# Kernel optimization log

Measured on AMD Instinct MI355X. Metric: run time of the kernel, lower is better.

Reference implementation:

```python
import jax, jax.numpy as jnp
import numpy as np

B, S, E = 2, 2048, 1024
HID = 1024
HEADS = 16
EPS = 1e-5
SCALE = (E * 2) ** (-0.5)  # source uses input_data_dim*2


def setup_inputs() -> dict:
    key = jax.random.key(0)
    k1, k2, k3 = jax.random.split(key, 3)
    return {
        "x": jax.random.normal(k1, (B, S, E), dtype=jnp.float32),
        "ln_g": jnp.ones((E,), jnp.float32),
        "ln_b": jnp.zeros((E,), jnp.float32),
        "W1": jax.random.normal(k2, (E, 3 * HID), jnp.float32) * 0.02,
        "b1": jnp.zeros((3 * HID,), jnp.float32),
        "W2": jax.random.normal(k3, (HID, HID), jnp.float32) * 0.02,
        "b2": jnp.zeros((HID,), jnp.float32),
    }


def reference(x, ln_g, ln_b, W1, b1, W2, b2):
    # LayerNorm over last dim
    mu = jnp.mean(x, axis=-1, keepdims=True)
    var = jnp.mean(jnp.square(x - mu), axis=-1, keepdims=True)
    xn = (x - mu) * jax.lax.rsqrt(var + EPS) * ln_g + ln_b
    # QKV projection: [B,S,3*HID]
    qkv = jnp.einsum('bse,ef->bsf', xn, W1) + b1
    # Faithful to source: flat reshape to (heads, B, S, 3*HID/heads)
    qkv_heads = qkv.reshape(HEADS, B, S, -1)
    q, k, v = jnp.split(qkv_heads, 3, axis=-1)  # each [H,B,S,d]
    scores = jnp.einsum('hbse,hbSe->hbsS', q, k) * SCALE  # [H,B,S,S]
    att = jax.nn.softmax(scores, axis=-1)
    full_att = jnp.einsum('hbsS,hbSe->hbse', att, v)  # [H,B,S,d]
    full_att = full_att.reshape(B, S, -1)  # faithful flat reshape -> [B,S,HID]
    out = jnp.einsum('bsh,hk->bsk', full_att, W2) + b2
    return out
```

## Files before the change

kernel.cpp:

```cpp
#include <hip/hip_runtime.h>

typedef unsigned short u16;
typedef __bf16 bf16x8 __attribute__((ext_vector_type(8)));
typedef float f32x4 __attribute__((ext_vector_type(4)));

static constexpr float SCALE2 = 0.022097086912079608f * 1.4426950408889634f;

__device__ __forceinline__ u16 f2b(float f) {
  union { float f; unsigned int i; } v; v.f = f;
  unsigned int r = v.i + 0x7fffu + ((v.i >> 16) & 1u);
  return (u16)(r >> 16);
}
__device__ __forceinline__ void async16(const u16* g, u16* l) {
  __builtin_amdgcn_global_load_lds((const __attribute__((address_space(1))) void*)g,
                                   (__attribute__((address_space(3))) void*)l,
                                   16, 0, 0);
}

__global__ __launch_bounds__(256) void ln_kernel(const float* __restrict__ x,
                                                 const float* __restrict__ g,
                                                 const float* __restrict__ b,
                                                 u16* __restrict__ xn) {
  const int row = blockIdx.x;
  const int t = threadIdx.x;
  float4 v = *(const float4*)(x + (size_t)row * 1024 + t * 4);
  float s = v.x + v.y + v.z + v.w;
  float ss = v.x * v.x + v.y * v.y + v.z * v.z + v.w * v.w;
  for (int off = 32; off >= 1; off >>= 1) {
    s += __shfl_xor(s, off, 64);
    ss += __shfl_xor(ss, off, 64);
  }
  __shared__ float red[8];
  const int w = t >> 6;
  if ((t & 63) == 0) { red[w] = s; red[4 + w] = ss; }
  __syncthreads();
  s = red[0] + red[1] + red[2] + red[3];
  ss = red[4] + red[5] + red[6] + red[7];
  const float mu = s * (1.0f / 1024.0f);
  const float var = ss * (1.0f / 1024.0f) - mu * mu;
  const float inv = rsqrtf(var + 1e-5f);
  float4 gg = *(const float4*)(g + t * 4);
  float4 bb = *(const float4*)(b + t * 4);
  ushort4 o;
  o.x = f2b((v.x - mu) * inv * gg.x + bb.x);
  o.y = f2b((v.y - mu) * inv * gg.y + bb.y);
  o.z = f2b((v.z - mu) * inv * gg.z + bb.z);
  o.w = f2b((v.w - mu) * inv * gg.w + bb.w);
  *(ushort4*)(xn + (size_t)row * 1024 + t * 4) = o;
}

__global__ void transpose_k(const float* __restrict__ in, u16* __restrict__ out,
                            int R, int C) {
  __shared__ float tile[32][33];
  const int c0 = blockIdx.x * 32, r0 = blockIdx.y * 32;
  const int tx = threadIdx.x, ty = threadIdx.y;
  for (int i = 0; i < 32; i += 8)
    tile[ty + i][tx] = in[(size_t)(r0 + ty + i) * C + c0 + tx];
  __syncthreads();
  for (int i = 0; i < 32; i += 8)
    out[(size_t)(c0 + ty + i) * R + r0 + tx] = f2b(tile[tx][ty + i]);
}

template <int MODE, int MT>
__global__ __launch_bounds__(256) void gemm_bt(const u16* __restrict__ A,
                                               const u16* __restrict__ Bt,
                                               const float* __restrict__ bias,
                                               float* __restrict__ C,
                                               int M, int N, int K,
                                               u16* __restrict__ Qc,
                                               u16* __restrict__ Kc,
                                               u16* __restrict__ Vtmp) {
  __shared__ __align__(16) u16 SMEM[8192];
  u16* As = SMEM;
  u16* Bs = SMEM + MT * 32;
  const int m0 = blockIdx.y * MT, n0 = blockIdx.x * 128;
  const int t = threadIdx.x, w = t >> 6, lane = t & 63;
  const int q = lane >> 4, l16 = lane & 15;
  const int wm = (w >> 1) * (MT / 2), wn = (w & 1) * 64;
  constexpr int NI = MT / 32;

  const int sc = (lane & 3) ^ ((lane >> 3) & 3);
  const u16* ap = A + (size_t)(m0 + w * 16 + (lane >> 2)) * K + sc * 8;
  const u16* bp = Bt + (size_t)(n0 + w * 16 + (lane >> 2)) * K + sc * 8;
  u16* lA = &As[w * 512];
  u16* lB = &Bs[w * 512];
  const int ac = q ^ ((l16 >> 1) & 3);

  f32x4 acc[NI][4];
  const f32x4 zero = {0.f, 0.f, 0.f, 0.f};
  for (int i = 0; i < NI; i++)
    for (int j = 0; j < 4; j++) acc[i][j] = zero;

  for (int k0 = 0; k0 < K; k0 += 32) {
    for (int i = 0; i < MT / 64; i++)
      async16(ap + (size_t)(i * 64) * K, lA + i * 2048);
    for (int i = 0; i < 2; i++)
      async16(bp + (size_t)(i * 64) * K, lB + i * 2048);
    ap += 32; bp += 32;
    __syncthreads();
    bf16x8 af[NI], bfr[4];
    for (int i = 0; i < NI; i++)
      af[i] = *(const bf16x8*)&As[(wm + i * 16 + l16) * 32 + ac * 8];
    for (int j = 0; j < 4; j++)
      bfr[j] = *(const bf16x8*)&Bs[(wn + j * 16 + l16) * 32 + ac * 8];
    for (int i = 0; i < NI; i++)
      for (int j = 0; j < 4; j++)
        acc[i][j] = __builtin_amdgcn_mfma_f32_16x16x32_bf16(af[i], bfr[j], acc[i][j], 0, 0, 0);
    __syncthreads();
  }

  if constexpr (MODE == 0) {
    for (int j = 0; j < 4; j++) {
      const int col = n0 + wn + j * 16 + l16;
      const float bv = bias[col];
      for (int i = 0; i < NI; i++) {
        const int rbase = m0 + wm + i * 16 + q * 4;
        for (int r = 0; r < 4; r++)
          C[(size_t)(rbase + r) * N + col] = acc[i][j][r] + bv;
      }
    }
  } else {
    const int seg = n0 + wn;
    const int k64 = seg >> 6;
    const int tcol = k64 / 3;
    const int typ = k64 - tcol * 3;
    u16* dst = (typ == 0) ? Qc : (typ == 1) ? Kc : Vtmp;
    const int gidx = m0 >> 7;
    u16* tw = &SMEM[w * 1280];
    float bv[4];
    for (int j = 0; j < 4; j++) bv[j] = bias[seg + j * 16 + l16];
    __syncthreads();
    for (int i = 0; i < 4; i++) {
      for (int j = 0; j < 4; j++) {
        ushort4 pk;
        pk.x = f2b(acc[i][j][0] + bv[j]);
        pk.y = f2b(acc[i][j][1] + bv[j]);
        pk.z = f2b(acc[i][j][2] + bv[j]);
        pk.w = f2b(acc[i][j][3] + bv[j]);
        *(ushort4*)&tw[(j * 16 + l16) * 20 + q * 4] = pk;
      }
      const int r2 = lane >> 2;
      const int quarter = lane & 3;
      u16 vals[16];
      for (int c = 0; c < 16; c++)
        vals[c] = tw[(quarter * 16 + c) * 20 + r2];
      const int lr = wm + i * 16 + r2;
      const int s = (lr << 4) + tcol;
      u16* dp = dst + ((size_t)gidx * 2048 + s) * 64 + quarter * 16;
      *(uint4*)&dp[0] = *(uint4*)&vals[0];
      *(uint4*)&dp[8] = *(uint4*)&vals[8];
    }
  }
}

__global__ __launch_bounds__(256) void vtrans(const u16* __restrict__ Vtmp,
                                              u16* __restrict__ Vt) {
  __shared__ __align__(16) u16 tile[64 * 64];
  const int g = blockIdx.y, s0 = blockIdx.x * 64;
  const int t = threadIdx.x;
  const int row = t >> 3, ch = t & 7;
  for (int p = 0; p < 2; p++) {
    const int r = p * 32 + row;
    uint4 v = *(const uint4*)&Vtmp[((size_t)g * 2048 + s0 + r) * 64 + ch * 8];
    *(uint4*)&tile[r * 64 + ((ch ^ (r & 7)) * 8)] = v;
  }
  __syncthreads();
  const int d = t >> 2, scn = t & 3;
  u16 vals[16];
  for (int j2 = 0; j2 < 16; j2++) {
    const int s = scn * 16 + j2;
    vals[j2] = tile[s * 64 + (((d >> 3) ^ (s & 7)) * 8) + (d & 7)];
  }
  u16* dp = Vt + ((size_t)g * 64 + d) * 2048 + s0 + scn * 16;
  *(uint4*)&dp[0] = *(uint4*)&vals[0];
  *(uint4*)&dp[8] = *(uint4*)&vals[8];
}

__global__ __launch_bounds__(256) void attn_kernel(const u16* __restrict__ Qc,
                                                   const u16* __restrict__ Kc,
                                                   const u16* __restrict__ Vt,
                                                   u16* __restrict__ Oc) {
  __shared__ __align__(16) u16 Ks[128 * 64];
  __shared__ __align__(16) u16 Ps[4 * 2176];
  __shared__ __align__(16) u16 Vs[64 * 128];
  const int g = blockIdx.y;
  const int q0 = blockIdx.x * 64;
  const int t = threadIdx.x, w = t >> 6, lane = t & 63;
  const int q = lane >> 4, l16 = lane & 15;

  const u16* Qg = Qc + (size_t)g * 2048 * 64;
  const u16* Kg = Kc + (size_t)g * 2048 * 64;
  const u16* Vg = Vt + (size_t)g * 64 * 2048;

  bf16x8 aq[2];
  for (int ks = 0; ks < 2; ks++)
    aq[ks] = *(const bf16x8*)&Qg[(size_t)(q0 + w * 16 + l16) * 64 + ks * 32 + q * 8];

  f32x4 accO[4];
  const f32x4 zero = {0.f, 0.f, 0.f, 0.f};
  for (int c = 0; c < 4; c++) accO[c] = zero;
  float m2 = -1e30f, lsum = 0.f;

  const int kc = (lane & 7) ^ ((lane >> 3) & 7);
  const int vc = (lane & 15) ^ ((w * 4 + (lane >> 4)) & 7);
  const u16* kp = Kg + (size_t)(w * 8 + (lane >> 3)) * 64 + kc * 8;
  const u16* vp = Vg + (size_t)(w * 4 + (lane >> 4)) * 2048 + vc * 8;
  u16* lK = &Ks[w * 512];
  u16* lV = &Vs[w * 512];

  const int kch = q ^ (l16 & 7);

  for (int it = 0; it < 16; it++) {
    const int kt0 = it * 128;
    for (int i = 0; i < 4; i++) {
      async16(kp + (size_t)kt0 * 64 + i * 2048, lK + i * 2048);
      async16(vp + kt0 + (size_t)i * 32768, lV + i * 2048);
    }
    __syncthreads();

    f32x4 sa[8];
    for (int ct = 0; ct < 8; ct++) {
      bf16x8 bk0 = *(const bf16x8*)&Ks[(ct * 16 + l16) * 64 + kch * 8];
      bf16x8 bk1 = *(const bf16x8*)&Ks[(ct * 16 + l16) * 64 + (kch ^ 4) * 8];
      f32x4 a = zero;
      a = __builtin_amdgcn_mfma_f32_16x16x32_bf16(bk0, aq[0], a, 0, 0, 0);
      a = __builtin_amdgcn_mfma_f32_16x16x32_bf16(bk1, aq[1], a, 0, 0, 0);
      sa[ct] = a;
    }

    float mx = -1e30f;
    for (int ct = 0; ct < 8; ct++) {
      sa[ct] *= SCALE2;
      for (int r = 0; r < 4; r++) mx = fmaxf(mx, sa[ct][r]);
    }
    mx = fmaxf(mx, __shfl_xor(mx, 16, 64));
    mx = fmaxf(mx, __shfl_xor(mx, 32, 64));
    const float mnew = fmaxf(m2, mx);
    const float alpha = __builtin_amdgcn_exp2f(m2 - mnew);
    m2 = mnew;

    u16* Pr = &Ps[w * 2176 + l16 * 136];
    f32x4 psv = zero;
    for (int ct = 0; ct < 8; ct++) {
      f32x4 p;
      for (int r = 0; r < 4; r++) p[r] = __builtin_amdgcn_exp2f(sa[ct][r] - mnew);
      psv += p;
      ushort4 pk;
      pk.x = f2b(p[0]); pk.y = f2b(p[1]); pk.z = f2b(p[2]); pk.w = f2b(p[3]);
      *(ushort4*)&Pr[ct * 16 + q * 4] = pk;
    }
    float psum = psv[0] + psv[1] + psv[2] + psv[3];
    psum += __shfl_xor(psum, 16, 64);
    psum += __shfl_xor(psum, 32, 64);
    lsum = lsum * alpha + psum;
    for (int c = 0; c < 4; c++) accO[c] *= alpha;

    u16* Psw = &Ps[w * 2176];
    for (int ks2 = 0; ks2 < 4; ks2++) {
      bf16x8 apf = *(const bf16x8*)&Psw[l16 * 136 + ks2 * 32 + q * 8];
      for (int c = 0; c < 4; c++) {
        const int vch = (ks2 * 4 + q) ^ (l16 & 7);
        bf16x8 bv = *(const bf16x8*)&Vs[(c * 16 + l16) * 128 + vch * 8];
        accO[c] = __builtin_amdgcn_mfma_f32_16x16x32_bf16(bv, apf, accO[c], 0, 0, 0);
      }
    }
    __syncthreads();
  }

  const int srow = q0 + w * 16 + l16;
  const int orow = g * 128 + (srow >> 4);
  const int cbase = (srow & 15) * 64;
  const float linv = 1.0f / lsum;
  for (int c = 0; c < 4; c++) {
    ushort4 o;
    o.x = f2b(accO[c][0] * linv);
    o.y = f2b(accO[c][1] * linv);
    o.z = f2b(accO[c][2] * linv);
    o.w = f2b(accO[c][3] * linv);
    *(ushort4*)&Oc[(size_t)orow * 1024 + cbase + c * 16 + q * 4] = o;
  }
}

extern "C" void kernel_launch(void* const* d_in, const int* in_sizes, int n_in,
                              void* d_out, int out_size, void* d_ws, size_t ws_size,
                              hipStream_t stream) {
  (void)in_sizes; (void)n_in; (void)out_size; (void)ws_size;
  const float* x    = (const float*)d_in[0];
  const float* ln_g = (const float*)d_in[1];
  const float* ln_b = (const float*)d_in[2];
  const float* W1   = (const float*)d_in[3];
  const float* b1   = (const float*)d_in[4];
  const float* W2   = (const float*)d_in[5];
  const float* b2   = (const float*)d_in[6];

  char* ws = (char*)d_ws;
  u16* xn   = (u16*)(ws);
  u16* W1T  = (u16*)(ws + ((size_t)8 << 20));
  u16* W2T  = (u16*)(ws + ((size_t)14 << 20));
  u16* Qc   = (u16*)(ws + ((size_t)16 << 20));
  u16* Kc   = (u16*)(ws + ((size_t)24 << 20));
  u16* Vtmp = (u16*)(ws + ((size_t)32 << 20));
  u16* Vt   = (u16*)(ws + ((size_t)40 << 20));
  u16* Oc   = xn;

  ln_kernel<<<dim3(4096), dim3(256), 0, stream>>>(x, ln_g, ln_b, xn);
  transpose_k<<<dim3(96, 32), dim3(32, 8), 0, stream>>>(W1, W1T, 1024, 3072);
  transpose_k<<<dim3(32, 32), dim3(32, 8), 0, stream>>>(W2, W2T, 1024, 1024);
  gemm_bt<1, 128><<<dim3(24, 32), dim3(256), 0, stream>>>(xn, W1T, b1, nullptr,
                                                          4096, 3072, 1024, Qc, Kc, Vtmp);
  vtrans<<<dim3(32, 32), dim3(256), 0, stream>>>(Vtmp, Vt);
  attn_kernel<<<dim3(32, 32), dim3(256), 0, stream>>>(Qc, Kc, Vt, Oc);
  gemm_bt<0, 64><<<dim3(8, 64), dim3(256), 0, stream>>>(Oc, W2T, b2, (float*)d_out,
                                                        4096, 1024, 1024, nullptr, nullptr, nullptr);
}
```

Baseline: 230.8 us.

## Double query rows per attention block and merge weight transposes into one kernel

```diff
diff --git a/kernel.cpp b/kernel.cpp
--- a/kernel.cpp
+++ b/kernel.cpp
@@ -49,16 +49,32 @@
   *(ushort4*)(xn + (size_t)row * 1024 + t * 4) = o;
 }
 
-__global__ void transpose_k(const float* __restrict__ in, u16* __restrict__ out,
-                            int R, int C) {
-  __shared__ float tile[32][33];
-  const int c0 = blockIdx.x * 32, r0 = blockIdx.y * 32;
-  const int tx = threadIdx.x, ty = threadIdx.y;
-  for (int i = 0; i < 32; i += 8)
-    tile[ty + i][tx] = in[(size_t)(r0 + ty + i) * C + c0 + tx];
+__global__ __launch_bounds__(256) void transpose2_k(const float* __restrict__ W1,
+                                                    u16* __restrict__ W1T,
+                                                    const float* __restrict__ W2,
+                                                    u16* __restrict__ W2T) {
+  const int z = blockIdx.z;
+  if (z == 1 && blockIdx.x >= 16) return;
+  const int C = z ? 1024 : 3072;
+  const float* in = z ? W2 : W1;
+  u16* out = z ? W2T : W1T;
+  __shared__ u16 tile[64 * 72];
+  const int c0 = blockIdx.x * 64, r0 = blockIdx.y * 64;
+  const int t = threadIdx.x;
+  const int row = t >> 2, cseg = t & 3;
+  for (int it = 0; it < 4; it++) {
+    float4 v = *(const float4*)&in[(size_t)(r0 + row) * C + c0 + it * 16 + cseg * 4];
+    ushort4 o;
+    o.x = f2b(v.x); o.y = f2b(v.y); o.z = f2b(v.z); o.w = f2b(v.w);
+    *(ushort4*)&tile[row * 72 + it * 16 + cseg * 4] = o;
+  }
   __syncthreads();
-  for (int i = 0; i < 32; i += 8)
-    out[(size_t)(c0 + ty + i) * R + r0 + tx] = f2b(tile[tx][ty + i]);
+  const int orow = t >> 2, ch = t & 3;
+  u16 vals[16];
+  for (int j = 0; j < 16; j++) vals[j] = tile[(ch * 16 + j) * 72 + orow];
+  u16* dp = out + (size_t)(c0 + orow) * 1024 + r0 + ch * 16;
+  *(uint4*)&dp[0] = *(uint4*)&vals[0];
+  *(uint4*)&dp[8] = *(uint4*)&vals[8];
 }
 
 template <int MODE, int MT>
@@ -180,11 +196,12 @@
                                                    const u16* __restrict__ Kc,
                                                    const u16* __restrict__ Vt,
                                                    u16* __restrict__ Oc) {
-  __shared__ __align__(16) u16 Ks[128 * 64];
-  __shared__ __align__(16) u16 Ps[4 * 2176];
-  __shared__ __align__(16) u16 Vs[64 * 128];
+  __shared__ __align__(16) u16 LDS[32768];
+  u16* Ks = LDS;
+  u16* Vs = LDS + 8192;
+  u16* Ps = LDS + 16384;
   const int g = blockIdx.y;
-  const int q0 = blockIdx.x * 64;
+  const int q0 = blockIdx.x * 128;
   const int t = threadIdx.x, w = t >> 6, lane = t & 63;
   const int q = lane >> 4, l16 = lane & 15;
 
@@ -192,14 +209,16 @@
   const u16* Kg = Kc + (size_t)g * 2048 * 64;
   const u16* Vg = Vt + (size_t)g * 64 * 2048;
 
-  bf16x8 aq[2];
-  for (int ks = 0; ks < 2; ks++)
-    aq[ks] = *(const bf16x8*)&Qg[(size_t)(q0 + w * 16 + l16) * 64 + ks * 32 + q * 8];
-
-  f32x4 accO[4];
+  bf16x8 aq[2][2];
+  for (int rt = 0; rt < 2; rt++)
+    for (int ks = 0; ks < 2; ks++)
+      aq[rt][ks] = *(const bf16x8*)&Qg[(size_t)(q0 + w * 32 + rt * 16 + l16) * 64 + ks * 32 + q * 8];
+
+  f32x4 accO[2][4];
   const f32x4 zero = {0.f, 0.f, 0.f, 0.f};
-  for (int c = 0; c < 4; c++) accO[c] = zero;
-  float m2 = -1e30f, lsum = 0.f;
+  for (int rt = 0; rt < 2; rt++)
+    for (int c = 0; c < 4; c++) accO[rt][c] = zero;
+  float m2[2] = {-1e30f, -1e30f}, lsum[2] = {0.f, 0.f};
 
   const int kc = (lane & 7) ^ ((lane >> 3) & 7);
   const int vc = (lane & 15) ^ ((w * 4 + (lane >> 4)) & 7);
@@ -209,6 +228,8 @@
   u16* lV = &Vs[w * 512];
 
   const int kch = q ^ (l16 & 7);
+  const int pbase = w * 4096;
+  const int pxor = l16 & 3;
 
   for (int it = 0; it < 16; it++) {
     const int kt0 = it * 128;
@@ -218,66 +239,74 @@
     }
     __syncthreads();
 
-    f32x4 sa[8];
+    f32x4 sa[2][8];
     for (int ct = 0; ct < 8; ct++) {
       bf16x8 bk0 = *(const bf16x8*)&Ks[(ct * 16 + l16) * 64 + kch * 8];
       bf16x8 bk1 = *(const bf16x8*)&Ks[(ct * 16 + l16) * 64 + (kch ^ 4) * 8];
-      f32x4 a = zero;
-      a = __builtin_amdgcn_mfma_f32_16x16x32_bf16(bk0, aq[0], a, 0, 0, 0);
-      a = __builtin_amdgcn_mfma_f32_16x16x32_bf16(bk1, aq[1], a, 0, 0, 0);
-      sa[ct] = a;
-    }
-
-    float mx = -1e30f;
-    for (int ct = 0; ct < 8; ct++) {
-      sa[ct] *= SCALE2;
-      for (int r = 0; r < 4; r++) mx = fmaxf(mx, sa[ct][r]);
-    }
-    mx = fmaxf(mx, __shfl_xor(mx, 16, 64));
-    mx = fmaxf(mx, __shfl_xor(mx, 32, 64));
-    const float mnew = fmaxf(m2, mx);
-    const float alpha = __builtin_amdgcn_exp2f(m2 - mnew);
-    m2 = mnew;
-
-    u16* Pr = &Ps[w * 2176 + l16 * 136];
-    f32x4 psv = zero;
-    for (int ct = 0; ct < 8; ct++) {
-      f32x4 p;
-      for (int r = 0; r < 4; r++) p[r] = __builtin_amdgcn_exp2f(sa[ct][r] - mnew);
-      psv += p;
-      ushort4 pk;
-      pk.x = f2b(p[0]); pk.y = f2b(p[1]); pk.z = f2b(p[2]); pk.w = f2b(p[3]);
-      *(ushort4*)&Pr[ct * 16 + q * 4] = pk;
-    }
-    float psum = psv[0] + psv[1] + psv[2] + psv[3];
-    psum += __shfl_xor(psum, 16, 64);
-    psum += __shfl_xor(psum, 32, 64);
-    lsum = lsum * alpha + psum;
-    for (int c = 0; c < 4; c++) accO[c] *= alpha;
-
-    u16* Psw = &Ps[w * 2176];
+      for (int rt = 0; rt < 2; rt++) {
+        f32x4 a = zero;
+        a = __builtin_amdgcn_mfma_f32_16x16x32_bf16(bk0, aq[rt][0], a, 0, 0, 0);
+        a = __builtin_amdgcn_mfma_f32_16x16x32_bf16(bk1, aq[rt][1], a, 0, 0, 0);
+        sa[rt][ct] = a;
+      }
+    }
+
+    for (int rt = 0; rt < 2; rt++) {
+      float mx = -1e30f;
+      for (int ct = 0; ct < 8; ct++) {
+        sa[rt][ct] *= SCALE2;
+        for (int r = 0; r < 4; r++) mx = fmaxf(mx, sa[rt][ct][r]);
+      }
+      mx = fmaxf(mx, __shfl_xor(mx, 16, 64));
+      mx = fmaxf(mx, __shfl_xor(mx, 32, 64));
+      const float mnew = fmaxf(m2[rt], mx);
+      const float alpha = __builtin_amdgcn_exp2f(m2[rt] - mnew);
+      m2[rt] = mnew;
+      const int sbase = pbase + rt * 2048 + l16 * 32;
+      f32x4 psv = zero;
+      for (int ct = 0; ct < 8; ct++) {
+        f32x4 p;
+        for (int r = 0; r < 4; r++) p[r] = __builtin_amdgcn_exp2f(sa[rt][ct][r] - mnew);
+        psv += p;
+        ushort4 pk;
+        pk.x = f2b(p[0]); pk.y = f2b(p[1]); pk.z = f2b(p[2]); pk.w = f2b(p[3]);
+        const int c2 = ((ct & 1) * 2 + (q >> 1)) ^ pxor;
+        *(ushort4*)&Ps[sbase + (ct >> 1) * 512 + c2 * 8 + (q & 1) * 4] = pk;
+      }
+      float psum = psv[0] + psv[1] + psv[2] + psv[3];
+      psum += __shfl_xor(psum, 16, 64);
+      psum += __shfl_xor(psum, 32, 64);
+      lsum[rt] = lsum[rt] * alpha + psum;
+      for (int c = 0; c < 4; c++) accO[rt][c] *= alpha;
+    }
+
     for (int ks2 = 0; ks2 < 4; ks2++) {
-      bf16x8 apf = *(const bf16x8*)&Psw[l16 * 136 + ks2 * 32 + q * 8];
+      bf16x8 apf[2];
+      for (int rt = 0; rt < 2; rt++)
+        apf[rt] = *(const bf16x8*)&Ps[pbase + rt * 2048 + ks2 * 512 + l16 * 32 + (ks2 * 0 + (q ^ pxor)) * 8];
       for (int c = 0; c < 4; c++) {
         const int vch = (ks2 * 4 + q) ^ (l16 & 7);
         bf16x8 bv = *(const bf16x8*)&Vs[(c * 16 + l16) * 128 + vch * 8];
-        accO[c] = __builtin_amdgcn_mfma_f32_16x16x32_bf16(bv, apf, accO[c], 0, 0, 0);
-      }
-    }
-    __syncthreads();
-  }
-
-  const int srow = q0 + w * 16 + l16;
-  const int orow = g * 128 + (srow >> 4);
-  const int cbase = (srow & 15) * 64;
-  const float linv = 1.0f / lsum;
-  for (int c = 0; c < 4; c++) {
-    ushort4 o;
-    o.x = f2b(accO[c][0] * linv);
-    o.y = f2b(accO[c][1] * linv);
-    o.z = f2b(accO[c][2] * linv);
-    o.w = f2b(accO[c][3] * linv);
-    *(ushort4*)&Oc[(size_t)orow * 1024 + cbase + c * 16 + q * 4] = o;
+        for (int rt = 0; rt < 2; rt++)
+          accO[rt][c] = __builtin_amdgcn_mfma_f32_16x16x32_bf16(bv, apf[rt], accO[rt][c], 0, 0, 0);
+      }
+    }
+    __syncthreads();
+  }
+
+  for (int rt = 0; rt < 2; rt++) {
+    const int srow = q0 + w * 32 + rt * 16 + l16;
+    const int orow = g * 128 + (srow >> 4);
+    const int cbase = (srow & 15) * 64;
+    const float linv = 1.0f / lsum[rt];
+    for (int c = 0; c < 4; c++) {
+      ushort4 o;
+      o.x = f2b(accO[rt][c][0] * linv);
+      o.y = f2b(accO[rt][c][1] * linv);
+      o.z = f2b(accO[rt][c][2] * linv);
+      o.w = f2b(accO[rt][c][3] * linv);
+      *(ushort4*)&Oc[(size_t)orow * 1024 + cbase + c * 16 + q * 4] = o;
+    }
   }
 }
 
@@ -304,12 +333,11 @@
   u16* Oc   = xn;
 
   ln_kernel<<<dim3(4096), dim3(256), 0, stream>>>(x, ln_g, ln_b, xn);
-  transpose_k<<<dim3(96, 32), dim3(32, 8), 0, stream>>>(W1, W1T, 1024, 3072);
-  transpose_k<<<dim3(32, 32), dim3(32, 8), 0, stream>>>(W2, W2T, 1024, 1024);
+  transpose2_k<<<dim3(48, 16, 2), dim3(256), 0, stream>>>(W1, W1T, W2, W2T);
   gemm_bt<1, 128><<<dim3(24, 32), dim3(256), 0, stream>>>(xn, W1T, b1, nullptr,
                                                           4096, 3072, 1024, Qc, Kc, Vtmp);
   vtrans<<<dim3(32, 32), dim3(256), 0, stream>>>(Vtmp, Vt);
-  attn_kernel<<<dim3(32, 32), dim3(256), 0, stream>>>(Qc, Kc, Vt, Oc);
+  attn_kernel<<<dim3(16, 32), dim3(256), 0, stream>>>(Qc, Kc, Vt, Oc);
   gemm_bt<0, 64><<<dim3(8, 64), dim3(256), 0, stream>>>(Oc, W2T, b2, (float*)d_out,
                                                         4096, 1024, 1024, nullptr, nullptr, nullptr);
 }
```

Measured after the change: 220.9 us. 1.04x faster.
